# Optimization experiments

Hardware: AMD Instinct MI355X
Metric: run time of the kernel (lower is better)

The kernel has to match this reference:

```python
import jax, jax.numpy as jnp
import numpy as np

C, P, H, W, BS = 256, 2, 128, 128, 4
NH, DH = 16, 16
NPATCH = (H // P) * (W // P)   # 4096
NTOK = NPATCH + 1              # 4097 with cls token
NMASK = int((1 - 0.75) * NTOK) # 1024 kept (visible) tokens
PRED = 512
NUM_BLOCKS = 1

def _sincos_pos_embed(embed_dim, h, w):
    # faithful port of get_2d_sincos_pos_embed
    def emb1d(d, pos):
        omega = np.arange(d // 2, dtype=np.float64) / (d / 2.0)
        omega = 1.0 / 10000 ** omega
        out = np.einsum('m,d->md', pos.reshape(-1), omega)
        return np.concatenate([np.sin(out), np.cos(out)], axis=1)
    gh = np.arange(h, dtype=np.float32)
    gw = np.arange(w, dtype=np.float32)
    grid = np.stack(np.meshgrid(gw, gh), axis=0).reshape(2, 1, h, w)
    emb = np.concatenate([emb1d(embed_dim // 2, grid[0]), emb1d(embed_dim // 2, grid[1])], axis=1)
    return jnp.asarray(emb, jnp.float32)  # [h*w, embed_dim]

def _ln(x, g, b, eps=1e-5):
    mu = x.mean(-1, keepdims=True)
    var = ((x - mu) ** 2).mean(-1, keepdims=True)
    return (x - mu) * jax.lax.rsqrt(var + eps) * g + b

def _gelu(x):
    return jax.nn.gelu(x, approximate=False)  # torch nn.GELU default (erf)

def _attn(x, qkv_w, qkv_b, proj_w, proj_b, nq_g, nq_b, nk_g, nk_b):
    bs, n, c = x.shape
    qkv = x @ qkv_w + qkv_b
    q, k, v = jnp.split(qkv, 3, axis=-1)
    heads = lambda t: t.reshape(bs, n, NH, DH).transpose(0, 2, 1, 3)  # [b,h,n,d]
    q, k, v = heads(q), heads(k), heads(v)
    q = _ln(q, nq_g, nq_b)  # per-head-dim QK LayerNorm
    k = _ln(k, nk_g, nk_b)
    score = jnp.einsum('bhnd,bhmd->bhnm', q, k) / np.float32(np.sqrt(DH))
    attn = jax.nn.softmax(score, axis=-1)
    attn_map = attn.mean(axis=1)[:, 0, 1:]  # [b, n-1]
    out = jnp.einsum('bhnm,bhmd->bhnd', attn, v)
    out = out.transpose(0, 2, 1, 3).reshape(bs, n, c)
    return out @ proj_w + proj_b, attn_map

def _forward(mask_index, x, Wp, bp, cls, qkv_w, qkv_b, proj_w, proj_b, nq_g, nq_b, nk_g, nk_b,
             conv_w, conv_b, ca1_w, ca1_b, ca2_w, ca2_b, mlp1_w, mlp1_b, mlp2_w, mlp2_b,
             node_w, ln0_g, ln0_b, h1_w, h1_b, ln1_g, ln1_b, h2_w, h2_b, ln2_g, ln2_b,
             h3_w, h3_b, pr_w, pr_b):
    bs = x.shape[0]
    # PatchEmbed: conv stride=kernel=P expressed as reshape + einsum
    xp = x.reshape(bs, 3, H // P, P, W // P, P)
    tok = jnp.einsum('bchpwq,ocpq->bohw', xp, Wp) + bp[None, :, None, None]
    tok = tok.reshape(bs, C, NPATCH).transpose(0, 2, 1)  # [b, l, c]
    tok = tok + _sincos_pos_embed(C, H // P, W // P)[None]
    tok = jnp.concatenate([jnp.broadcast_to(cls, (bs, 1, C)), tok], axis=1)  # prepend cls
    # mask_img: keep NMASK tokens per the precomputed permutation prefix
    m = jnp.take_along_axis(tok, mask_index[:, :, None], axis=1)  # [b, NMASK, C]

    attn_map = None
    for blk in range(NUM_BLOCKS):
        feat = m[..., None]  # feature_list: [b, l, c, width]
        for i in range(4):
            j = blk * 4 + i
            xl = feat[..., -1]
            o1 = _gelu(xl @ conv_w[j] + conv_b[j])  # Conv1x1Act
            gate = jax.nn.sigmoid(jax.nn.relu(xl @ ca1_w[j] + ca1_b[j]) @ ca2_w[j] + ca2_b[j])
            o2 = gate * xl                           # ChannelAttention
            o4 = _gelu(xl @ mlp1_w[j] + mlp1_b[j]) @ mlp2_w[j] + mlp2_b[j]  # MLP
            cat = jnp.concatenate([feat, jnp.stack([o1, o2, xl, o4], axis=-1)], axis=-1)  # width 5+i
            wmix = jax.nn.softmax(node_w[j, :5 + i] / 0.01)
            mixed = jnp.einsum('blcn,n->blc', cat, wmix)
            a_out, attn_map = _attn(mixed, qkv_w[j], qkv_b[j], proj_w[j], proj_b[j],
                                    nq_g[j], nq_b[j], nk_g[j], nk_b[j])
            xo = a_out + mixed  # residual
            feat = jnp.concatenate([feat, xo[..., None]], axis=-1)
        m = xo
    # Predict_head (tokenwise)
    h = _ln(m, ln0_g, ln0_b)
    h = h @ h1_w + h1_b
    h = _ln(h, ln1_g, ln1_b)
    h = h @ h2_w + h2_b
    h = _ln(h, ln2_g, ln2_b)
    h = h @ h3_w + h3_b
    return h @ pr_w + pr_b  # [b, NMASK, PRED]

def setup_inputs():
    key = jax.random.key(0)
    ks = iter(jax.random.split(key, 64))
    rn = lambda shape, s=0.02: jax.random.normal(next(ks), shape, jnp.float32) * s
    noise = jax.random.normal(next(ks), (BS, NTOK))
    mask_index = jnp.argsort(noise, axis=-1)[:, :NMASK].astype(jnp.int32)
    return dict(
        x=jax.random.normal(next(ks), (BS, 3, H, W), jnp.float32),
        mask_index=mask_index,
        Wp=rn((C, 3, P, P)), bp=jnp.zeros((C,)), cls=rn((1, 1, C)),
        qkv_w=rn((4, C, 3 * C)), qkv_b=jnp.zeros((4, 3 * C)),
        proj_w=rn((4, C, C)), proj_b=jnp.zeros((4, C)),
        nq_g=jnp.ones((4, DH)), nq_b=jnp.zeros((4, DH)),
        nk_g=jnp.ones((4, DH)), nk_b=jnp.zeros((4, DH)),
        conv_w=rn((4, C, C)), conv_b=jnp.zeros((4, C)),
        ca1_w=rn((4, C, C // 16)), ca1_b=jnp.zeros((4, C // 16)),
        ca2_w=rn((4, C // 16, C)), ca2_b=jnp.zeros((4, C)),
        mlp1_w=rn((4, C, 4 * C)), mlp1_b=jnp.zeros((4, 4 * C)),
        mlp2_w=rn((4, 4 * C, C)), mlp2_b=jnp.zeros((4, C)),
        node_w=jax.random.normal(next(ks), (4, 8), jnp.float32),
        ln0_g=jnp.ones((C,)), ln0_b=jnp.zeros((C,)),
        h1_w=rn((C, 2048)), h1_b=jnp.zeros((2048,)),
        ln1_g=jnp.ones((2048,)), ln1_b=jnp.zeros((2048,)),
        h2_w=rn((2048, 256)), h2_b=jnp.zeros((256,)),
        ln2_g=jnp.ones((256,)), ln2_b=jnp.zeros((256,)),
        h3_w=rn((256, 2048)), h3_b=jnp.zeros((2048,)),
        pr_w=rn((2048, PRED)), pr_b=jnp.zeros((PRED,)),
    )

def reference(x, mask_index, Wp, bp, cls, qkv_w, qkv_b, proj_w, proj_b, nq_g, nq_b, nk_g, nk_b,
              conv_w, conv_b, ca1_w, ca1_b, ca2_w, ca2_b, mlp1_w, mlp1_b, mlp2_w, mlp2_b,
              node_w, ln0_g, ln0_b, h1_w, h1_b, ln1_g, ln1_b, h2_w, h2_b, ln2_g, ln2_b,
              h3_w, h3_b, pr_w, pr_b):
    return _forward(mask_index, x, Wp, bp, cls, qkv_w, qkv_b, proj_w, proj_b, nq_g, nq_b, nk_g, nk_b,
                    conv_w, conv_b, ca1_w, ca1_b, ca2_w, ca2_b, mlp1_w, mlp1_b, mlp2_w, mlp2_b,
                    node_w, ln0_g, ln0_b, h1_w, h1_b, ln1_g, ln1_b, h2_w, h2_b, ln2_g, ln2_b,
                    h3_w, h3_b, pr_w, pr_b)
```

## Files before the change

### kernel.cpp

```cpp
#include <hip/hip_runtime.h>
#include <math.h>
#include <cstddef>

#define RTOK 4096
#define CDIM 256
#define NHEAD 16
#define DHEAD 16
#define SEQ 1024
#define BSZ 4

#define ACT_NONE 0
#define ACT_GELU 1

typedef short short8 __attribute__((ext_vector_type(8)));
typedef float f32x4  __attribute__((ext_vector_type(4)));
typedef _Float16 half8 __attribute__((ext_vector_type(8)));
typedef _Float16 half4 __attribute__((ext_vector_type(4)));

__device__ __forceinline__ float gelu_erf(float x) {
    return 0.5f * x * (1.0f + erff(x * 0.70710678118654752f));
}
__device__ __forceinline__ unsigned short f2b(float f) {
    unsigned u = __float_as_uint(f);
    unsigned r = (u + 0x7FFFu + ((u >> 16) & 1u)) >> 16;
    return (unsigned short)r;
}
__device__ __forceinline__ float b2f(unsigned short u) {
    return __uint_as_float((unsigned)u << 16);
}
__device__ __forceinline__ void gld16(const unsigned short* g, unsigned short* l) {
    __builtin_amdgcn_global_load_lds(
        (const __attribute__((address_space(1))) unsigned int*)g,
        (__attribute__((address_space(3))) unsigned int*)l, 16, 0, 0);
}
__device__ __forceinline__ float node_wsel(const float* nwp, int cnt, int widx) {
    float ww[8];
    float mx = -1e30f;
    for (int t = 0; t < cnt; ++t) { ww[t] = nwp[t] * 100.0f; mx = fmaxf(mx, ww[t]); }
    float ssum = 0.0f;
    for (int t = 0; t < cnt; ++t) { ww[t] = expf(ww[t] - mx); ssum += ww[t]; }
    return ww[widx] / ssum;
}

struct WtSeg { const float* in; unsigned short* out; int K, N, ntx, tpz, zin, zout; };
struct WtTab { WtSeg s[9]; int cum[10]; };

__global__ __launch_bounds__(256) void wtrans_all(WtTab tab)
{
    int g = blockIdx.x;
    int si = 0;
    #pragma unroll
    for (int i = 0; i < 8; ++i) if (g >= tab.cum[i + 1]) si = i + 1;
    WtSeg sg = tab.s[si];
    int t = g - tab.cum[si];
    int z = t / sg.tpz, r = t % sg.tpz;
    int kb = (r % sg.ntx) * 32, nb = (r / sg.ntx) * 32;
    const float* in = sg.in + (size_t)z * sg.zin;
    unsigned short* out = sg.out + (size_t)z * sg.zout;

    __shared__ float tt[32][33];
    int tx = threadIdx.x & 31, ty = threadIdx.x >> 5;
    #pragma unroll
    for (int rr = 0; rr < 4; ++rr) {
        int kk = ty * 4 + rr;
        tt[kk][tx] = in[(size_t)(kb + kk) * sg.N + nb + tx];
    }
    __syncthreads();
    #pragma unroll
    for (int rr = 0; rr < 4; ++rr) {
        int nn = ty * 4 + rr;
        out[(size_t)(nb + nn) * sg.K + kb + tx] = f2b(tt[tx][nn]);
    }
}

__global__ __launch_bounds__(256) void embed_kernel(
    const float* __restrict__ x, const int* __restrict__ mask_index,
    const float* __restrict__ Wp, const float* __restrict__ bp,
    const float* __restrict__ cls,
    float* __restrict__ out, unsigned short* __restrict__ outb)
{
    int row = blockIdx.x;
    int b = row >> 10;
    int c = threadIdx.x;
    int idx = mask_index[row];
    if (idx == 0) {
        float v = cls[c];
        out[(size_t)row * 256 + c] = v;
        outb[(size_t)row * 256 + c] = f2b(v);
        return;
    }
    int p  = idx - 1;
    int ph = p >> 6, pw = p & 63;

    __shared__ float xs[12];
    if (c < 12) {
        int ch = c >> 2, r = (c >> 1) & 1, q = c & 1;
        xs[c] = x[(((size_t)b * 3 + ch) * 128 + (ph * 2 + r)) * 128 + (pw * 2 + q)];
    }
    __syncthreads();

    float acc = bp[c];
    #pragma unroll
    for (int t = 0; t < 12; ++t) acc += xs[t] * Wp[c * 12 + t];

    int part = c >> 6, cc = c & 63;
    double omega = exp((double)cc * -0.14391156831212787);
    double posv  = (part < 2) ? (double)pw : (double)ph;
    double a     = posv * omega;
    double e     = ((part & 1) == 0) ? sin(a) : cos(a);
    float v = acc + (float)e;
    out[(size_t)row * 256 + c] = v;
    outb[(size_t)row * 256 + c] = f2b(v);
}

template<int MT, int ACT, bool RES, bool FOUT, int BMODE, bool SPLIT, int NW>
__global__ __launch_bounds__(256) void gemm_mfma(
    const unsigned short* __restrict__ A, const unsigned short* __restrict__ Bt,
    const float* __restrict__ bias, const float* __restrict__ bias1,
    const float* __restrict__ Rsd,
    float* __restrict__ C, unsigned short* __restrict__ Cb,
    int M, int N, int K, int N0,
    const float* __restrict__ nwp, int ncnt, int widx)
{
    constexpr int BM = 64 * MT;
    __shared__ __align__(16) unsigned short As0[BM * 64];
    __shared__ __align__(16) unsigned short As1[BM * 64];
    __shared__ __align__(16) unsigned short Bs0[64 * 64];
    __shared__ __align__(16) unsigned short Bs1[64 * 64];
    int tid = threadIdx.x;
    int w = tid >> 6, lane = tid & 63;
    int l15 = lane & 15, q = lane >> 4;

    int gx = gridDim.x, gy = gridDim.y;
    int L = blockIdx.x + gx * blockIdx.y;
    int xcd = L & 7, j = L >> 3;
    int by = xcd * (gy >> 3) + j / gx;
    int bx = j - (j / gx) * gx;
    int row0 = by * BM, col0 = bx * 64;

    f32x4 acc[MT][4];
    #pragma unroll
    for (int mt = 0; mt < MT; ++mt)
        #pragma unroll
        for (int nt = 0; nt < 4; ++nt)
            acc[mt][nt] = (f32x4){0.f, 0.f, 0.f, 0.f};

#define G_ISSUE(AS, BS, KB)                                                   \
    do {                                                                      \
        _Pragma("unroll")                                                     \
        for (int t = 0; t < 2 * MT; ++t) {                                    \
            int slot = tid + t * 256;                                         \
            int r = slot >> 3;                                                \
            int s = (slot & 7) ^ (r & 7);                                     \
            gld16(A + (size_t)(row0 + r) * K + (KB) + s * 8, &AS[slot * 8]);  \
        }                                                                     \
        _Pragma("unroll")                                                     \
        for (int t = 0; t < 2; ++t) {                                         \
            int slot = tid + t * 256;                                         \
            int r = slot >> 3;                                                \
            int s = (slot & 7) ^ (r & 7);                                     \
            gld16(Bt + (size_t)(col0 + r) * K + (KB) + s * 8, &BS[slot * 8]); \
        }                                                                     \
    } while (0)

#define G_COMPUTE(AS, BS)                                                     \
    do {                                                                      \
        _Pragma("unroll")                                                     \
        for (int hh = 0; hh < 2; ++hh) {                                      \
            short8 af[MT];                                                    \
            _Pragma("unroll")                                                 \
            for (int mt = 0; mt < MT; ++mt) {                                 \
                int R = w * 16 * MT + mt * 16 + l15;                          \
                int c = hh * 4 + q;                                           \
                af[mt] = *(const short8*)&AS[R * 64 + ((c ^ (R & 7)) << 3)];  \
            }                                                                 \
            _Pragma("unroll")                                                 \
            for (int nt = 0; nt < 4; ++nt) {                                  \
                int R = nt * 16 + l15;                                        \
                int c = hh * 4 + q;                                           \
                short8 bf = *(const short8*)&BS[R * 64 + ((c ^ (R & 7)) << 3)];\
                _Pragma("unroll")                                             \
                for (int mt = 0; mt < MT; ++mt)                               \
                    acc[mt][nt] = __builtin_amdgcn_mfma_f32_16x16x32_bf16(    \
                        af[mt], bf, acc[mt][nt], 0, 0, 0);                    \
            }                                                                 \
        }                                                                     \
    } while (0)

    G_ISSUE(As0, Bs0, 0);
    for (int kb = 0; kb < K; kb += 128) {
        __syncthreads();
        G_ISSUE(As1, Bs1, kb + 64);
        G_COMPUTE(As0, Bs0);
        __syncthreads();
        if (kb + 128 < K) G_ISSUE(As0, Bs0, kb + 128);
        G_COMPUTE(As1, Bs1);
    }
#undef G_ISSUE
#undef G_COMPUTE

    float wsel = 0.0f;
    if (NW > 0) wsel = node_wsel(nwp, ncnt, widx);

    #pragma unroll
    for (int mt = 0; mt < MT; ++mt) {
        #pragma unroll
        for (int nt = 0; nt < 4; ++nt) {
            #pragma unroll
            for (int reg = 0; reg < 4; ++reg) {
                int row = row0 + w * 16 * MT + mt * 16 + q * 4 + reg;
                int col = col0 + nt * 16 + l15;
                if (SPLIT) {
                    float v = acc[mt][nt][reg] +
                              (col < N0 ? bias[col] : bias1[col - N0]);
                    if (ACT == ACT_GELU) v = gelu_erf(v);
                    if (col < N0) {
                        if (NW == 1) C[(size_t)row * N0 + col] += wsel * v;
                        else         C[(size_t)row * N0 + col] = v;
                    } else {
                        Cb[(size_t)row * (N - N0) + (col - N0)] = f2b(v);
                    }
                } else {
                    float v = acc[mt][nt][reg] + bias[col];
                    if (ACT == ACT_GELU) v = gelu_erf(v);
                    if (NW == 2) v = wsel * v + Rsd[(size_t)row * N + col];
                    else if (RES) v += Rsd[(size_t)row * N + col];
                    if (FOUT) C[(size_t)row * N + col] = v;
                    if (BMODE == 1) Cb[(size_t)row * N + col] = f2b(v);
                    if (BMODE == 2) {
                        _Float16 hv = (_Float16)v;
                        Cb[(size_t)row * N + col] = *(unsigned short*)&hv;
                    }
                }
            }
        }
    }
}

__global__ __launch_bounds__(256) void chanattn_kernel(
    const float* __restrict__ xl,
    const float* f0, const float* f1, const float* f2,
    const float* __restrict__ ca1w, const float* __restrict__ ca1b,
    const float* __restrict__ ca2w, const float* __restrict__ ca2b,
    const float* __restrict__ node_w, int cnt,
    float* __restrict__ MIX)
{
    __shared__ float xs[256];
    __shared__ float sm16[16];
    size_t row = blockIdx.x;
    int tid = threadIdx.x;
    xs[tid] = xl[row * 256 + tid];
    __syncthreads();

    int h = tid >> 4, part = tid & 15;
    float p = 0.f;
    #pragma unroll
    for (int i = 0; i < 16; ++i)
        p += xs[part * 16 + i] * ca1w[(part * 16 + i) * 16 + h];
    p += __shfl_down(p, 8, 16);
    p += __shfl_down(p, 4, 16);
    p += __shfl_down(p, 2, 16);
    p += __shfl_down(p, 1, 16);
    if (part == 0) sm16[h] = fmaxf(p + ca1b[h], 0.0f);
    __syncthreads();

    float g = ca2b[tid];
    #pragma unroll
    for (int hh = 0; hh < 16; ++hh) g += sm16[hh] * ca2w[hh * 256 + tid];
    g = 1.0f / (1.0f + expf(-g));
    float o2 = g * xs[tid];

    float ww[8];
    float mx = -1e30f;
    for (int t = 0; t < cnt; ++t) { ww[t] = node_w[t] * 100.0f; mx = fmaxf(mx, ww[t]); }
    float ssum = 0.0f;
    for (int t = 0; t < cnt; ++t) { ww[t] = expf(ww[t] - mx); ssum += ww[t]; }
    float inv = 1.0f / ssum;
    int j = cnt - 5;
    float acc = (ww[j] + ww[j + 3]) * inv * xs[tid] + ww[j + 2] * inv * o2;
    const float* fs[3] = {f0, f1, f2};
    for (int t = 0; t < j; ++t) acc += ww[t] * inv * fs[t][row * 256 + tid];
    MIX[row * 256 + tid] = acc;
}

__global__ __launch_bounds__(256) void ln256_kernel(
    const float* __restrict__ in, unsigned short* __restrict__ outb,
    const float* __restrict__ g, const float* __restrict__ bb)
{
    int row = blockIdx.x * 4 + (threadIdx.x >> 6);
    int lane = threadIdx.x & 63;
    f32x4 xv = *(const f32x4*)(in + (size_t)row * 256 + lane * 4);
    float s = xv[0] + xv[1] + xv[2] + xv[3];
    #pragma unroll
    for (int off = 1; off < 64; off <<= 1) s += __shfl_xor(s, off, 64);
    float mu = s * (1.0f / 256.0f);
    float d0 = xv[0]-mu, d1 = xv[1]-mu, d2 = xv[2]-mu, d3 = xv[3]-mu;
    float s2 = d0*d0 + d1*d1 + d2*d2 + d3*d3;
    #pragma unroll
    for (int off = 1; off < 64; off <<= 1) s2 += __shfl_xor(s2, off, 64);
    float rstd = rsqrtf(s2 * (1.0f / 256.0f) + 1e-5f);
    f32x4 gv = *(const f32x4*)(g + lane * 4);
    f32x4 bv = *(const f32x4*)(bb + lane * 4);
    ushort4 o;
    o.x = f2b(d0 * rstd * gv[0] + bv[0]);
    o.y = f2b(d1 * rstd * gv[1] + bv[1]);
    o.z = f2b(d2 * rstd * gv[2] + bv[2]);
    o.w = f2b(d3 * rstd * gv[3] + bv[3]);
    *(ushort4*)(outb + (size_t)row * 256 + lane * 4) = o;
}

__global__ __launch_bounds__(256) void lnwb_kernel(
    const unsigned short* __restrict__ in, unsigned short* __restrict__ outb,
    const float* __restrict__ g, const float* __restrict__ bb, int N)
{
    __shared__ float sm[4];
    size_t row = blockIdx.x;
    const unsigned short* xr = in + row * N;
    int lane = threadIdx.x & 63, wid = threadIdx.x >> 6;

    float s = 0.0f;
    for (int i = threadIdx.x; i < N; i += 256) s += b2f(xr[i]);
    #pragma unroll
    for (int off = 32; off > 0; off >>= 1) s += __shfl_down(s, off, 64);
    if (lane == 0) sm[wid] = s;
    __syncthreads();
    float mu = (sm[0] + sm[1] + sm[2] + sm[3]) / N;
    __syncthreads();

    float s2 = 0.0f;
    for (int i = threadIdx.x; i < N; i += 256) { float d = b2f(xr[i]) - mu; s2 += d * d; }
    #pragma unroll
    for (int off = 32; off > 0; off >>= 1) s2 += __shfl_down(s2, off, 64);
    if (lane == 0) sm[wid] = s2;
    __syncthreads();
    float var = (sm[0] + sm[1] + sm[2] + sm[3]) / N;
    float rstd = rsqrtf(var + 1e-5f);

    for (int i = threadIdx.x; i < N; i += 256)
        outb[row * N + i] = f2b((b2f(xr[i]) - mu) * rstd * g[i] + bb[i]);
}

__global__ __launch_bounds__(256) void attn_prep(
    const unsigned short* __restrict__ qkvh,
    const float* __restrict__ nqg, const float* __restrict__ nqb,
    const float* __restrict__ nkg, const float* __restrict__ nkb,
    unsigned short* __restrict__ Qph, unsigned short* __restrict__ Kph,
    unsigned short* __restrict__ Vph)
{
    int b = blockIdx.x >> 6;
    int tokbase = (blockIdx.x & 63) * 16;
    int tid = threadIdx.x;
    int tl = tid >> 4, h = tid & 15;
    int tok = tokbase + tl;
    const _Float16* qkv = (const _Float16*)qkvh;
    const _Float16* rowp = qkv + ((size_t)(b * 1024 + tok)) * 768;
    _Float16* Qp = (_Float16*)Qph;
    _Float16* Kp = (_Float16*)Kph;
    _Float16* Vp = (_Float16*)Vph;
    const float QSC = 0.25f * 1.44269504088896340736f;

    __shared__ _Float16 vt[16][16][17];

    {
        half8 a0 = *(const half8*)(rowp + h * 16);
        half8 a1 = *(const half8*)(rowp + h * 16 + 8);
        float v[16];
        #pragma unroll
        for (int e = 0; e < 8; ++e) { v[e] = (float)a0[e]; v[8 + e] = (float)a1[e]; }
        float mu = 0.f;
        #pragma unroll
        for (int d = 0; d < 16; ++d) mu += v[d];
        mu *= (1.0f / 16.0f);
        float var = 0.f;
        #pragma unroll
        for (int d = 0; d < 16; ++d) { float t = v[d] - mu; var += t * t; }
        var *= (1.0f / 16.0f);
        float rstd = rsqrtf(var + 1e-5f);
        half8 o0, o1;
        #pragma unroll
        for (int e = 0; e < 8; ++e) {
            o0[e] = (_Float16)(((v[e] - mu) * rstd * nqg[e] + nqb[e]) * QSC);
            o1[e] = (_Float16)(((v[8+e] - mu) * rstd * nqg[8+e] + nqb[8+e]) * QSC);
        }
        _Float16* qo = Qp + ((size_t)(b * 16 + h) * 1024 + tok) * 16;
        *(half8*)qo = o0;
        *(half8*)(qo + 8) = o1;
    }
    {
        half8 a0 = *(const half8*)(rowp + 256 + h * 16);
        half8 a1 = *(const half8*)(rowp + 256 + h * 16 + 8);
        float v[16];
        #pragma unroll
        for (int e = 0; e < 8; ++e) { v[e] = (float)a0[e]; v[8 + e] = (float)a1[e]; }
        float mu = 0.f;
        #pragma unroll
        for (int d = 0; d < 16; ++d) mu += v[d];
        mu *= (1.0f / 16.0f);
        float var = 0.f;
        #pragma unroll
        for (int d = 0; d < 16; ++d) { float t = v[d] - mu; var += t * t; }
        var *= (1.0f / 16.0f);
        float rstd = rsqrtf(var + 1e-5f);
        half8 o0, o1;
        #pragma unroll
        for (int e = 0; e < 8; ++e) {
            o0[e] = (_Float16)((v[e] - mu) * rstd * nkg[e] + nkb[e]);
            o1[e] = (_Float16)((v[8+e] - mu) * rstd * nkg[8+e] + nkb[8+e]);
        }
        _Float16* ko = Kp + ((size_t)(b * 16 + h) * 1024 + tok) * 16;
        *(half8*)ko = o0;
        *(half8*)(ko + 8) = o1;
    }
    {
        half8 a0 = *(const half8*)(rowp + 512 + h * 16);
        half8 a1 = *(const half8*)(rowp + 512 + h * 16 + 8);
        #pragma unroll
        for (int e = 0; e < 8; ++e) { vt[tl][h][e] = a0[e]; vt[tl][h][8 + e] = a1[e]; }
    }
    __syncthreads();
    {
        int h2 = tid >> 4, d = tid & 15;
        half8 o0, o1;
        #pragma unroll
        for (int t = 0; t < 8; ++t) { o0[t] = vt[t][h2][d]; o1[t] = vt[8 + t][h2][d]; }
        _Float16* vo = Vp + ((size_t)(b * 16 + h2) * 16 + d) * 1024 + tokbase;
        *(half8*)vo = o0;
        *(half8*)(vo + 8) = o1;
    }
}

__global__ __launch_bounds__(256) void attn_kernel(
    const unsigned short* __restrict__ Qph, const unsigned short* __restrict__ Kph,
    const unsigned short* __restrict__ Vph,
    unsigned short* __restrict__ outb)
{
    int qt = blockIdx.x, h = blockIdx.y, b = blockIdx.z;
    int bh = b * 16 + h;
    int tid = threadIdx.x;
    int w = tid >> 6, lane = tid & 63;
    int l15 = lane & 15, quad = lane >> 4;
    const _Float16* Qp = (const _Float16*)Qph + (size_t)bh * 1024 * 16;
    const _Float16* Kp = (const _Float16*)Kph + (size_t)bh * 1024 * 16;
    const _Float16* Vp = (const _Float16*)Vph + (size_t)bh * 16 * 1024;

    __shared__ __align__(16) _Float16 Qs[64 * 40];
    __shared__ __align__(16) _Float16 Kb[128 * 40];
    __shared__ __align__(16) _Float16 Vt[16 * 136];
    __shared__ __align__(16) _Float16 Ps[4][16 * 136];

    uint4 z4 = {0, 0, 0, 0};
    if (tid < 64) {
        *(uint4*)&Qs[tid * 40 + 16] = z4;
        *(uint4*)&Qs[tid * 40 + 24] = z4;
    } else if (tid < 192) {
        int r = tid - 64;
        *(uint4*)&Kb[r * 40 + 16] = z4;
        *(uint4*)&Kb[r * 40 + 24] = z4;
    }
    if (tid < 128) {
        int r = tid >> 1, part = tid & 1;
        *(uint4*)&Qs[r * 40 + part * 8] =
            *(const uint4*)(Qp + (size_t)(qt * 64 + r) * 16 + part * 8);
    }
    __syncthreads();

    half8 bq = *(const half8*)&Qs[(w * 16 + l15) * 40 + quad * 8];
    float mst = -1e30f, lst = 0.f;
    f32x4 acco = (f32x4){0.f, 0.f, 0.f, 0.f};

    for (int kt = 0; kt < 8; ++kt) {
        __syncthreads();
        {
            int r = tid >> 1, part = tid & 1;
            *(uint4*)&Kb[r * 40 + part * 8] =
                *(const uint4*)(Kp + (size_t)(kt * 128 + r) * 16 + part * 8);
        }
        {
            int d = tid >> 4, kk8 = tid & 15;
            *(uint4*)&Vt[d * 136 + kk8 * 8] =
                *(const uint4*)(Vp + (size_t)d * 1024 + kt * 128 + kk8 * 8);
        }
        __syncthreads();

        f32x4 sacc[8];
        #pragma unroll
        for (int ni = 0; ni < 8; ++ni) {
            half8 ak = *(const half8*)&Kb[(ni * 16 + l15) * 40 + quad * 8];
            sacc[ni] = __builtin_amdgcn_mfma_f32_16x16x32_f16(
                ak, bq, (f32x4){0.f, 0.f, 0.f, 0.f}, 0, 0, 0);
        }
        half8 bv[4];
        #pragma unroll
        for (int c = 0; c < 4; ++c)
            bv[c] = *(const half8*)&Vt[l15 * 136 + c * 32 + quad * 8];

        float rm = sacc[0][0];
        #pragma unroll
        for (int ni = 0; ni < 8; ++ni)
            #pragma unroll
            for (int reg = 0; reg < 4; ++reg)
                rm = fmaxf(rm, sacc[ni][reg]);
        rm = fmaxf(rm, __shfl_xor(rm, 16, 64));
        rm = fmaxf(rm, __shfl_xor(rm, 32, 64));
        float mn  = fmaxf(mst, rm);
        float cor = exp2f(mst - mn);
        mst = mn;
        lst *= cor;
        #pragma unroll
        for (int reg = 0; reg < 4; ++reg) {
            float cR = __shfl(cor, (lane & 48) + quad * 4 + reg, 64);
            acco[reg] *= cR;
        }
        float lsum = 0.f;
        #pragma unroll
        for (int ni = 0; ni < 8; ++ni) {
            half4 ph;
            #pragma unroll
            for (int reg = 0; reg < 4; ++reg) {
                float p = exp2f(sacc[ni][reg] - mn);
                lsum += p;
                ph[reg] = (_Float16)p;
            }
            *(half4*)&Ps[w][l15 * 136 + ni * 16 + quad * 4] = ph;
        }
        lsum += __shfl_xor(lsum, 16, 64);
        lsum += __shfl_xor(lsum, 32, 64);
        lst += lsum;

        #pragma unroll
        for (int c = 0; c < 4; ++c) {
            half8 p0 = *(const half8*)&Ps[w][l15 * 136 + c * 32 + quad * 8];
            acco = __builtin_amdgcn_mfma_f32_16x16x32_f16(p0, bv[c], acco, 0, 0, 0);
        }
    }

    #pragma unroll
    for (int reg = 0; reg < 4; ++reg) {
        float lR = __shfl(lst, (lane & 48) + quad * 4 + reg, 64);
        float o = acco[reg] / lR;
        int row = b * 1024 + qt * 64 + w * 16 + quad * 4 + reg;
        outb[(size_t)row * 256 + h * 16 + l15] = f2b(o);
    }
}

extern "C" void kernel_launch(void* const* d_in, const int* in_sizes, int n_in,
                              void* d_out, int out_size, void* d_ws, size_t ws_size,
                              hipStream_t stream)
{
    const float* x          = (const float*)d_in[0];
    const int*   mask_index = (const int*)  d_in[1];
    const float* Wp         = (const float*)d_in[2];
    const float* bp         = (const float*)d_in[3];
    const float* cls        = (const float*)d_in[4];
    const float* qkv_w      = (const float*)d_in[5];
    const float* qkv_b      = (const float*)d_in[6];
    const float* proj_w     = (const float*)d_in[7];
    const float* proj_b     = (const float*)d_in[8];
    const float* nq_g       = (const float*)d_in[9];
    const float* nq_b       = (const float*)d_in[10];
    const float* nk_g       = (const float*)d_in[11];
    const float* nk_b       = (const float*)d_in[12];
    const float* conv_w     = (const float*)d_in[13];
    const float* conv_b     = (const float*)d_in[14];
    const float* ca1_w      = (const float*)d_in[15];
    const float* ca1_b      = (const float*)d_in[16];
    const float* ca2_w      = (const float*)d_in[17];
    const float* ca2_b      = (const float*)d_in[18];
    const float* mlp1_w     = (const float*)d_in[19];
    const float* mlp1_b     = (const float*)d_in[20];
    const float* mlp2_w     = (const float*)d_in[21];
    const float* mlp2_b     = (const float*)d_in[22];
    const float* node_w     = (const float*)d_in[23];
    const float* ln0_g      = (const float*)d_in[24];
    const float* ln0_b      = (const float*)d_in[25];
    const float* h1_w       = (const float*)d_in[26];
    const float* h1_b       = (const float*)d_in[27];
    const float* ln1_g      = (const float*)d_in[28];
    const float* ln1_b      = (const float*)d_in[29];
    const float* h2_w       = (const float*)d_in[30];
    const float* h2_b       = (const float*)d_in[31];
    const float* ln2_g      = (const float*)d_in[32];
    const float* ln2_b      = (const float*)d_in[33];
    const float* h3_w       = (const float*)d_in[34];
    const float* h3_b       = (const float*)d_in[35];
    const float* pr_w       = (const float*)d_in[36];
    const float* pr_b       = (const float*)d_in[37];
    float* out = (float*)d_out;

    char* base = (char*)d_ws;
    size_t off = 0;
    auto alloc = [&](size_t bytes) -> char* {
        char* p = base + off;
        off += (bytes + 255) & ~(size_t)255;
        return p;
    };
    const size_t RC = (size_t)RTOK * CDIM;
    float* F[5];
    unsigned short* Fb[5];
    for (int i = 0; i < 5; ++i) F[i] = (float*)alloc(RC * 4);
    for (int i = 0; i < 5; ++i) Fb[i] = (unsigned short*)alloc(RC * 2);
    float* MIX = (float*)alloc(RC * 4);
    unsigned short* MIXb = (unsigned short*)alloc(RC * 2);
    unsigned short* AOb  = (unsigned short*)alloc(RC * 2);
    unsigned short* BIGH = (unsigned short*)alloc((size_t)RTOK * 768 * 2);
    unsigned short* Qp   = (unsigned short*)alloc(RC * 2);
    unsigned short* Kp   = (unsigned short*)alloc(RC * 2);
    unsigned short* Vp   = (unsigned short*)alloc(RC * 2);
    unsigned short* H1b  = (unsigned short*)alloc((size_t)RTOK * 2048 * 2);
    unsigned short* MIDU = (unsigned short*)alloc((size_t)RTOK * 2048 * 2);
    unsigned short* L0b  = (unsigned short*)alloc(RC * 2);
    unsigned short* L2b  = (unsigned short*)alloc(RC * 2);
    unsigned short* H3b  = (unsigned short*)alloc((size_t)RTOK * 2048 * 2);
    unsigned short* cm1b  = (unsigned short*)alloc((size_t)4 * 1280 * 256 * 2);
    unsigned short* qkvb  = (unsigned short*)alloc((size_t)4 * 768 * 256 * 2);
    unsigned short* projb = (unsigned short*)alloc((size_t)4 * 256 * 256 * 2);
    unsigned short* mlp2b = (unsigned short*)alloc((size_t)4 * 256 * 1024 * 2);
    unsigned short* h1b   = (unsigned short*)alloc((size_t)2048 * 256 * 2);
    unsigned short* h2b   = (unsigned short*)alloc((size_t)256 * 2048 * 2);
    unsigned short* h3b   = (unsigned short*)alloc((size_t)2048 * 256 * 2);
    unsigned short* prb   = (unsigned short*)alloc((size_t)512 * 2048 * 2);

    {
        WtTab tab;
        int c = 0, idx = 0;
        auto seg = [&](const float* in, unsigned short* outp, int K, int N,
                       int z, int zin, int zout) {
            WtSeg s; s.in = in; s.out = outp; s.K = K; s.N = N;
            s.ntx = K / 32; s.tpz = (K / 32) * (N / 32);
            s.zin = zin; s.zout = zout;
            tab.s[idx] = s; tab.cum[idx] = c;
            c += s.tpz * z; ++idx;
        };
        seg(conv_w, cm1b,         256, 256,  4, 256 * 256,  1280 * 256);
        seg(mlp1_w, cm1b + 65536, 256, 1024, 4, 256 * 1024, 1280 * 256);
        seg(qkv_w,  qkvb,  256, 768,  4, 256 * 768,  768 * 256);
        seg(proj_w, projb, 256, 256,  4, 256 * 256,  256 * 256);
        seg(mlp2_w, mlp2b, 1024, 256, 4, 1024 * 256, 256 * 1024);
        seg(h1_w, h1b, 256, 2048, 1, 0, 0);
        seg(h2_w, h2b, 2048, 256, 1, 0, 0);
        seg(h3_w, h3b, 256, 2048, 1, 0, 0);
        seg(pr_w, prb, 2048, 512, 1, 0, 0);
        tab.cum[9] = c;
        wtrans_all<<<c, 256, 0, stream>>>(tab);
    }

    embed_kernel<<<RTOK, 256, 0, stream>>>(x, mask_index, Wp, bp, cls, F[0], Fb[0]);

    for (int j = 0; j < 4; ++j) {
        const float* xl = F[j];
        const unsigned short* xlb = Fb[j];
        chanattn_kernel<<<RTOK, 256, 0, stream>>>(
            xl, F[0], F[1], F[2],
            ca1_w + (size_t)j * 256 * 16, ca1_b + j * 16,
            ca2_w + (size_t)j * 16 * 256, ca2_b + j * 256,
            node_w + j * 8, 5 + j, MIX);
        gemm_mfma<2, ACT_GELU, false, false, 0, true, 1><<<dim3(20, 32), 256, 0, stream>>>(
            xlb, cm1b + (size_t)j * 1280 * 256, conv_b + j * 256, mlp1_b + j * 1024,
            nullptr, MIX, MIDU, RTOK, 1280, 256, 256, node_w + j * 8, 5 + j, j + 1);
        gemm_mfma<1, ACT_NONE, false, true, 1, false, 2><<<dim3(4, 64), 256, 0, stream>>>(
            MIDU, mlp2b + (size_t)j * 256 * 1024, mlp2_b + j * 256, nullptr, MIX,
            MIX, MIXb, RTOK, 256, 1024, 0, node_w + j * 8, 5 + j, j + 4);
        gemm_mfma<2, ACT_NONE, false, false, 2, false, 0><<<dim3(12, 32), 256, 0, stream>>>(
            MIXb, qkvb + (size_t)j * 768 * 256, qkv_b + j * 768, nullptr, nullptr,
            nullptr, BIGH, RTOK, 768, 256, 0, nullptr, 0, 0);
        attn_prep<<<256, 256, 0, stream>>>(
            BIGH, nq_g + j * 16, nq_b + j * 16, nk_g + j * 16, nk_b + j * 16,
            Qp, Kp, Vp);
        attn_kernel<<<dim3(16, NHEAD, BSZ), 256, 0, stream>>>(Qp, Kp, Vp, AOb);
        gemm_mfma<1, ACT_NONE, true, true, 1, false, 0><<<dim3(4, 64), 256, 0, stream>>>(
            AOb, projb + (size_t)j * 256 * 256, proj_b + j * 256, nullptr, MIX,
            F[j + 1], Fb[j + 1], RTOK, 256, 256, 0, nullptr, 0, 0);
    }

    ln256_kernel<<<1024, 256, 0, stream>>>(F[4], L0b, ln0_g, ln0_b);
    gemm_mfma<2, ACT_NONE, false, false, 1, false, 0><<<dim3(32, 32), 256, 0, stream>>>(
        L0b, h1b, h1_b, nullptr, nullptr, nullptr, H1b, RTOK, 2048, 256, 0,
        nullptr, 0, 0);
    lnwb_kernel<<<RTOK, 256, 0, stream>>>(H1b, MIDU, ln1_g, ln1_b, 2048);
    gemm_mfma<1, ACT_NONE, false, true, 0, false, 0><<<dim3(4, 64), 256, 0, stream>>>(
        MIDU, h2b, h2_b, nullptr, nullptr, MIX, nullptr, RTOK, 256, 2048, 0,
        nullptr, 0, 0);
    ln256_kernel<<<1024, 256, 0, stream>>>(MIX, L2b, ln2_g, ln2_b);
    gemm_mfma<2, ACT_NONE, false, false, 1, false, 0><<<dim3(32, 32), 256, 0, stream>>>(
        L2b, h3b, h3_b, nullptr, nullptr, nullptr, H3b, RTOK, 2048, 256, 0,
        nullptr, 0, 0);
    gemm_mfma<1, ACT_NONE, false, true, 0, false, 0><<<dim3(8, 64), 256, 0, stream>>>(
        H3b, prb, pr_b, nullptr, nullptr, out, nullptr, RTOK, 512, 2048, 0,
        nullptr, 0, 0);
}
```

Measured before the change: 671.6 us.

## Merge setup kernels, fuse conv/mlp1 GEMM with channel attention, pipeline attention loads

Merges the weight-transpose and embedding kernels into one launch. It also runs the conv+mlp1 GEMM and the channel-attention kernel as two block ranges of a single launch, writing the conv branch to a separate O1 buffer that the mlp2 GEMM epilogue folds into MIX. The LayerNorm over 2048 columns now uses one wavefront per row with vector loads and shuffle reductions. The attention kernel double-buffers K/V tiles in registers and LDS and switches QK to the 16x16x16 f16 MFMA with compact layouts. These changes aim to cut launch count, serial dependencies and LDS sync stalls, at the cost of an extra fp32 buffer and more epilogue reads.

```diff
diff --git a/kernel.cpp b/kernel.cpp
--- a/kernel.cpp
+++ b/kernel.cpp
@@ -45,72 +45,68 @@
 struct WtSeg { const float* in; unsigned short* out; int K, N, ntx, tpz, zin, zout; };
 struct WtTab { WtSeg s[9]; int cum[10]; };
 
-__global__ __launch_bounds__(256) void wtrans_all(WtTab tab)
-{
-    int g = blockIdx.x;
-    int si = 0;
-    #pragma unroll
-    for (int i = 0; i < 8; ++i) if (g >= tab.cum[i + 1]) si = i + 1;
-    WtSeg sg = tab.s[si];
-    int t = g - tab.cum[si];
-    int z = t / sg.tpz, r = t % sg.tpz;
-    int kb = (r % sg.ntx) * 32, nb = (r / sg.ntx) * 32;
-    const float* in = sg.in + (size_t)z * sg.zin;
-    unsigned short* out = sg.out + (size_t)z * sg.zout;
-
-    __shared__ float tt[32][33];
-    int tx = threadIdx.x & 31, ty = threadIdx.x >> 5;
-    #pragma unroll
-    for (int rr = 0; rr < 4; ++rr) {
-        int kk = ty * 4 + rr;
-        tt[kk][tx] = in[(size_t)(kb + kk) * sg.N + nb + tx];
-    }
-    __syncthreads();
-    #pragma unroll
-    for (int rr = 0; rr < 4; ++rr) {
-        int nn = ty * 4 + rr;
-        out[(size_t)(nb + nn) * sg.K + kb + tx] = f2b(tt[tx][nn]);
-    }
-}
-
-__global__ __launch_bounds__(256) void embed_kernel(
+__global__ __launch_bounds__(256) void setup_kernel(
+    WtTab tab,
     const float* __restrict__ x, const int* __restrict__ mask_index,
     const float* __restrict__ Wp, const float* __restrict__ bp,
     const float* __restrict__ cls,
-    float* __restrict__ out, unsigned short* __restrict__ outb)
+    float* __restrict__ Fout, unsigned short* __restrict__ Fbout)
 {
-    int row = blockIdx.x;
-    int b = row >> 10;
-    int c = threadIdx.x;
-    int idx = mask_index[row];
-    if (idx == 0) {
-        float v = cls[c];
-        out[(size_t)row * 256 + c] = v;
-        outb[(size_t)row * 256 + c] = f2b(v);
-        return;
-    }
-    int p  = idx - 1;
-    int ph = p >> 6, pw = p & 63;
-
+    __shared__ float tt[32][33];
     __shared__ float xs[12];
-    if (c < 12) {
-        int ch = c >> 2, r = (c >> 1) & 1, q = c & 1;
-        xs[c] = x[(((size_t)b * 3 + ch) * 128 + (ph * 2 + r)) * 128 + (pw * 2 + q)];
-    }
-    __syncthreads();
-
-    float acc = bp[c];
-    #pragma unroll
-    for (int t = 0; t < 12; ++t) acc += xs[t] * Wp[c * 12 + t];
-
-    int part = c >> 6, cc = c & 63;
-    double omega = exp((double)cc * -0.14391156831212787);
-    double posv  = (part < 2) ? (double)pw : (double)ph;
-    double a     = posv * omega;
-    double e     = ((part & 1) == 0) ? sin(a) : cos(a);
-    float v = acc + (float)e;
-    out[(size_t)row * 256 + c] = v;
-    outb[(size_t)row * 256 + c] = f2b(v);
+    if ((int)blockIdx.x < tab.cum[9]) {
+        int g = blockIdx.x;
+        int si = 0;
+        #pragma unroll
+        for (int i = 0; i < 8; ++i) if (g >= tab.cum[i + 1]) si = i + 1;
+        WtSeg sg = tab.s[si];
+        int t = g - tab.cum[si];
+        int z = t / sg.tpz, r = t % sg.tpz;
+        int kb = (r % sg.ntx) * 32, nb = (r / sg.ntx) * 32;
+        const float* in = sg.in + (size_t)z * sg.zin;
+        unsigned short* out = sg.out + (size_t)z * sg.zout;
+        int tx = threadIdx.x & 31, ty = threadIdx.x >> 5;
+        #pragma unroll
+        for (int rr = 0; rr < 4; ++rr) {
+            int kk = ty * 4 + rr;
+            tt[kk][tx] = in[(size_t)(kb + kk) * sg.N + nb + tx];
+        }
+        __syncthreads();
+        #pragma unroll
+        for (int rr = 0; rr < 4; ++rr) {
+            int nn = ty * 4 + rr;
+            out[(size_t)(nb + nn) * sg.K + kb + tx] = f2b(tt[tx][nn]);
+        }
+    } else {
+        int row = blockIdx.x - tab.cum[9];
+        int b = row >> 10;
+        int c = threadIdx.x;
+        int idx = mask_index[row];
+        if (idx == 0) {
+            float v = cls[c];
+            Fout[(size_t)row * 256 + c] = v;
+            Fbout[(size_t)row * 256 + c] = f2b(v);
+            return;
+        }
+        int p  = idx - 1;
+        int ph = p >> 6, pw = p & 63;
+        if (c < 12) {
+            int ch = c >> 2, r = (c >> 1) & 1, q = c & 1;
+            xs[c] = x[(((size_t)b * 3 + ch) * 128 + (ph * 2 + r)) * 128 + (pw * 2 + q)];
+        }
+        __syncthreads();
+        float acc = bp[c];
+        #pragma unroll
+        for (int t = 0; t < 12; ++t) acc += xs[t] * Wp[c * 12 + t];
+        int part = c >> 6, cc = c & 63;
+        double omega = exp((double)cc * -0.14391156831212787);
+        double posv  = (part < 2) ? (double)pw : (double)ph;
+        double a     = posv * omega;
+        double e     = ((part & 1) == 0) ? sin(a) : cos(a);
+        float v = acc + (float)e;
+        Fout[(size_t)row * 256 + c] = v;
+        Fbout[(size_t)row * 256 + c] = f2b(v);
+    }
 }
 
 template<int MT, int ACT, bool RES, bool FOUT, int BMODE, bool SPLIT, int NW>
@@ -120,7 +116,8 @@
     const float* __restrict__ Rsd,
     float* __restrict__ C, unsigned short* __restrict__ Cb,
     int M, int N, int K, int N0,
-    const float* __restrict__ nwp, int ncnt, int widx)
+    const float* __restrict__ nwp, int ncnt, int widx,
+    const float* __restrict__ O1p, int widxB)
 {
     constexpr int BM = 64 * MT;
     __shared__ __align__(16) unsigned short As0[BM * 64];
@@ -199,8 +196,9 @@
 #undef G_ISSUE
 #undef G_COMPUTE
 
-    float wsel = 0.0f;
+    float wsel = 0.0f, wselB = 0.0f;
     if (NW > 0) wsel = node_wsel(nwp, ncnt, widx);
+    if (NW == 4) wselB = node_wsel(nwp, ncnt, widxB);
 
     #pragma unroll
     for (int mt = 0; mt < MT; ++mt) {
@@ -214,16 +212,14 @@
                     float v = acc[mt][nt][reg] +
                               (col < N0 ? bias[col] : bias1[col - N0]);
                     if (ACT == ACT_GELU) v = gelu_erf(v);
-                    if (col < N0) {
-                        if (NW == 1) C[(size_t)row * N0 + col] += wsel * v;
-                        else         C[(size_t)row * N0 + col] = v;
-                    } else {
-                        Cb[(size_t)row * (N - N0) + (col - N0)] = f2b(v);
-                    }
+                    if (col < N0) C[(size_t)row * N0 + col] = v;
+                    else Cb[(size_t)row * (N - N0) + (col - N0)] = f2b(v);
                 } else {
                     float v = acc[mt][nt][reg] + bias[col];
                     if (ACT == ACT_GELU) v = gelu_erf(v);
                     if (NW == 2) v = wsel * v + Rsd[(size_t)row * N + col];
+                    else if (NW == 4) v = wsel * v + Rsd[(size_t)row * N + col]
+                                        + wselB * O1p[(size_t)row * N + col];
                     else if (RES) v += Rsd[(size_t)row * N + col];
                     if (FOUT) C[(size_t)row * N + col] = v;
                     if (BMODE == 1) Cb[(size_t)row * N + col] = f2b(v);
@@ -237,7 +233,10 @@
     }
 }
 
-__global__ __launch_bounds__(256) void chanattn_kernel(
+__global__ __launch_bounds__(256) void cm1chan_kernel(
+    const unsigned short* __restrict__ A, const unsigned short* __restrict__ Bt,
+    const float* __restrict__ biasC, const float* __restrict__ biasM,
+    float* __restrict__ O1, unsigned short* __restrict__ MIDU,
     const float* __restrict__ xl,
     const float* f0, const float* f1, const float* f2,
     const float* __restrict__ ca1w, const float* __restrict__ ca1b,
@@ -245,42 +244,138 @@
     const float* __restrict__ node_w, int cnt,
     float* __restrict__ MIX)
 {
+    __shared__ __align__(16) unsigned short As0[128 * 64];
+    __shared__ __align__(16) unsigned short As1[128 * 64];
+    __shared__ __align__(16) unsigned short Bs0[64 * 64];
+    __shared__ __align__(16) unsigned short Bs1[64 * 64];
     __shared__ float xs[256];
     __shared__ float sm16[16];
-    size_t row = blockIdx.x;
     int tid = threadIdx.x;
-    xs[tid] = xl[row * 256 + tid];
-    __syncthreads();
-
-    int h = tid >> 4, part = tid & 15;
-    float p = 0.f;
-    #pragma unroll
-    for (int i = 0; i < 16; ++i)
-        p += xs[part * 16 + i] * ca1w[(part * 16 + i) * 16 + h];
-    p += __shfl_down(p, 8, 16);
-    p += __shfl_down(p, 4, 16);
-    p += __shfl_down(p, 2, 16);
-    p += __shfl_down(p, 1, 16);
-    if (part == 0) sm16[h] = fmaxf(p + ca1b[h], 0.0f);
-    __syncthreads();
-
-    float g = ca2b[tid];
-    #pragma unroll
-    for (int hh = 0; hh < 16; ++hh) g += sm16[hh] * ca2w[hh * 256 + tid];
-    g = 1.0f / (1.0f + expf(-g));
-    float o2 = g * xs[tid];
-
-    float ww[8];
-    float mx = -1e30f;
-    for (int t = 0; t < cnt; ++t) { ww[t] = node_w[t] * 100.0f; mx = fmaxf(mx, ww[t]); }
-    float ssum = 0.0f;
-    for (int t = 0; t < cnt; ++t) { ww[t] = expf(ww[t] - mx); ssum += ww[t]; }
-    float inv = 1.0f / ssum;
-    int j = cnt - 5;
-    float acc = (ww[j] + ww[j + 3]) * inv * xs[tid] + ww[j + 2] * inv * o2;
-    const float* fs[3] = {f0, f1, f2};
-    for (int t = 0; t < j; ++t) acc += ww[t] * inv * fs[t][row * 256 + tid];
-    MIX[row * 256 + tid] = acc;
+
+    if ((int)blockIdx.x < 640) {
+        const int K = 256, N0 = 256;
+        int w = tid >> 6, lane = tid & 63;
+        int l15 = lane & 15, q = lane >> 4;
+        int L = blockIdx.x;
+        int xcd = L & 7, j = L >> 3;
+        int by = xcd * 4 + j / 20;
+        int bx = j - (j / 20) * 20;
+        int row0 = by * 128, col0 = bx * 64;
+
+        f32x4 acc[2][4];
+        #pragma unroll
+        for (int mt = 0; mt < 2; ++mt)
+            #pragma unroll
+            for (int nt = 0; nt < 4; ++nt)
+                acc[mt][nt] = (f32x4){0.f, 0.f, 0.f, 0.f};
+
+#define C_ISSUE(AS, BS, KB)                                                   \
+    do {                                                                      \
+        _Pragma("unroll")                                                     \
+        for (int t = 0; t < 4; ++t) {                                         \
+            int slot = tid + t * 256;                                         \
+            int r = slot >> 3;                                                \
+            int s = (slot & 7) ^ (r & 7);                                     \
+            gld16(A + (size_t)(row0 + r) * K + (KB) + s * 8, &AS[slot * 8]);  \
+        }                                                                     \
+        _Pragma("unroll")                                                     \
+        for (int t = 0; t < 2; ++t) {                                         \
+            int slot = tid + t * 256;                                         \
+            int r = slot >> 3;                                                \
+            int s = (slot & 7) ^ (r & 7);                                     \
+            gld16(Bt + (size_t)(col0 + r) * K + (KB) + s * 8, &BS[slot * 8]); \
+        }                                                                     \
+    } while (0)
+
+#define C_COMPUTE(AS, BS)                                                     \
+    do {                                                                      \
+        _Pragma("unroll")                                                     \
+        for (int hh = 0; hh < 2; ++hh) {                                      \
+            short8 af[2];                                                     \
+            _Pragma("unroll")                                                 \
+            for (int mt = 0; mt < 2; ++mt) {                                  \
+                int R = w * 32 + mt * 16 + l15;                               \
+                int c = hh * 4 + q;                                           \
+                af[mt] = *(const short8*)&AS[R * 64 + ((c ^ (R & 7)) << 3)];  \
+            }                                                                 \
+            _Pragma("unroll")                                                 \
+            for (int nt = 0; nt < 4; ++nt) {                                  \
+                int R = nt * 16 + l15;                                        \
+                int c = hh * 4 + q;                                           \
+                short8 bf = *(const short8*)&BS[R * 64 + ((c ^ (R & 7)) << 3)];\
+                _Pragma("unroll")                                             \
+                for (int mt = 0; mt < 2; ++mt)                                \
+                    acc[mt][nt] = __builtin_amdgcn_mfma_f32_16x16x32_bf16(    \
+                        af[mt], bf, acc[mt][nt], 0, 0, 0);                    \
+            }                                                                 \
+        }                                                                     \
+    } while (0)
+
+        C_ISSUE(As0, Bs0, 0);
+        for (int kb = 0; kb < K; kb += 128) {
+            __syncthreads();
+            C_ISSUE(As1, Bs1, kb + 64);
+            C_COMPUTE(As0, Bs0);
+            __syncthreads();
+            if (kb + 128 < K) C_ISSUE(As0, Bs0, kb + 128);
+            C_COMPUTE(As1, Bs1);
+        }
+#undef C_ISSUE
+#undef C_COMPUTE
+
+        #pragma unroll
+        for (int mt = 0; mt < 2; ++mt) {
+            #pragma unroll
+            for (int nt = 0; nt < 4; ++nt) {
+                #pragma unroll
+                for (int reg = 0; reg < 4; ++reg) {
+                    int row = row0 + w * 32 + mt * 16 + q * 4 + reg;
+                    int col = col0 + nt * 16 + l15;
+                    if (col < N0) {
+                        float v = gelu_erf(acc[mt][nt][reg] + biasC[col]);
+                        O1[(size_t)row * 256 + col] = v;
+                    } else {
+                        float v = gelu_erf(acc[mt][nt][reg] + biasM[col - 256]);
+                        MIDU[(size_t)row * 1024 + (col - 256)] = f2b(v);
+                    }
+                }
+            }
+        }
+    } else {
+        size_t row = blockIdx.x - 640;
+        xs[tid] = xl[row * 256 + tid];
+        __syncthreads();
+
+        int h = tid >> 4, part = tid & 15;
+        float p = 0.f;
+        #pragma unroll
+        for (int i = 0; i < 16; ++i)
+            p += xs[part * 16 + i] * ca1w[(part * 16 + i) * 16 + h];
+        p += __shfl_down(p, 8, 16);
+        p += __shfl_down(p, 4, 16);
+        p += __shfl_down(p, 2, 16);
+        p += __shfl_down(p, 1, 16);
+        if (part == 0) sm16[h] = fmaxf(p + ca1b[h], 0.0f);
+        __syncthreads();
+
+        float g = ca2b[tid];
+        #pragma unroll
+        for (int hh = 0; hh < 16; ++hh) g += sm16[hh] * ca2w[hh * 256 + tid];
+        g = 1.0f / (1.0f + expf(-g));
+        float o2 = g * xs[tid];
+
+        float ww[8];
+        float mx = -1e30f;
+        for (int t = 0; t < cnt; ++t) { ww[t] = node_w[t] * 100.0f; mx = fmaxf(mx, ww[t]); }
+        float ssum = 0.0f;
+        for (int t = 0; t < cnt; ++t) { ww[t] = expf(ww[t] - mx); ssum += ww[t]; }
+        float inv = 1.0f / ssum;
+        int jj = cnt - 5;
+        float acc2 = (ww[jj] + ww[jj + 3]) * inv * xs[tid] + ww[jj + 2] * inv * o2;
+        const float* fs[3] = {f0, f1, f2};
+        for (int t = 0; t < jj; ++t) acc2 += ww[t] * inv * fs[t][row * 256 + tid];
+        MIX[row * 256 + tid] = acc2;
+    }
 }
 
 __global__ __launch_bounds__(256) void ln256_kernel(
@@ -309,35 +404,39 @@
     *(ushort4*)(outb + (size_t)row * 256 + lane * 4) = o;
 }
 
-__global__ __launch_bounds__(256) void lnwb_kernel(
+__global__ __launch_bounds__(256) void ln2048w_kernel(
     const unsigned short* __restrict__ in, unsigned short* __restrict__ outb,
-    const float* __restrict__ g, const float* __restrict__ bb, int N)
+    const float* __restrict__ g, const float* __restrict__ bb)
 {
-    __shared__ float sm[4];
-    size_t row = blockIdx.x;
-    const unsigned short* xr = in + row * N;
-    int lane = threadIdx.x & 63, wid = threadIdx.x >> 6;
-
-    float s = 0.0f;
-    for (int i = threadIdx.x; i < N; i += 256) s += b2f(xr[i]);
-    #pragma unroll
-    for (int off = 32; off > 0; off >>= 1) s += __shfl_down(s, off, 64);
-    if (lane == 0) sm[wid] = s;
-    __syncthreads();
-    float mu = (sm[0] + sm[1] + sm[2] + sm[3]) / N;
-    __syncthreads();
-
-    float s2 = 0.0f;
-    for (int i = threadIdx.x; i < N; i += 256) { float d = b2f(xr[i]) - mu; s2 += d * d; }
-    #pragma unroll
-    for (int off = 32; off > 0; off >>= 1) s2 += __shfl_down(s2, off, 64);
-    if (lane == 0) sm[wid] = s2;
-    __syncthreads();
-    float var = (sm[0] + sm[1] + sm[2] + sm[3]) / N;
-    float rstd = rsqrtf(var + 1e-5f);
-
-    for (int i = threadIdx.x; i < N; i += 256)
-        outb[row * N + i] = f2b((b2f(xr[i]) - mu) * rstd * g[i] + bb[i]);
+    int row = blockIdx.x * 4 + (threadIdx.x >> 6);
+    int lane = threadIdx.x & 63;
+    const unsigned short* xr = in + (size_t)row * 2048 + lane * 32;
+    unsigned short v[32];
+    *(uint4*)&v[0]  = *(const uint4*)&xr[0];
+    *(uint4*)&v[8]  = *(const uint4*)&xr[8];
+    *(uint4*)&v[16] = *(const uint4*)&xr[16];
+    *(uint4*)&v[24] = *(const uint4*)&xr[24];
+    float s = 0.f;
+    #pragma unroll
+    for (int i = 0; i < 32; ++i) s += b2f(v[i]);
+    #pragma unroll
+    for (int off = 1; off < 64; off <<= 1) s += __shfl_xor(s, off, 64);
+    float mu = s * (1.0f / 2048.0f);
+    float s2 = 0.f;
+    #pragma unroll
+    for (int i = 0; i < 32; ++i) { float d = b2f(v[i]) - mu; s2 += d * d; }
+    #pragma unroll
+    for (int off = 1; off < 64; off <<= 1) s2 += __shfl_xor(s2, off, 64);
+    float rstd = rsqrtf(s2 * (1.0f / 2048.0f) + 1e-5f);
+    unsigned short o[32];
+    #pragma unroll
+    for (int i = 0; i < 32; ++i)
+        o[i] = f2b((b2f(v[i]) - mu) * rstd * g[lane * 32 + i] + bb[lane * 32 + i]);
+    unsigned short* op = outb + (size_t)row * 2048 + lane * 32;
+    *(uint4*)&op[0]  = *(const uint4*)&o[0];
+    *(uint4*)&op[8]  = *(const uint4*)&o[8];
+    *(uint4*)&op[16] = *(const uint4*)&o[16];
+    *(uint4*)&op[24] = *(const uint4*)&o[24];
 }
 
 __global__ __launch_bounds__(256) void attn_prep(
@@ -443,56 +542,65 @@
     const _Float16* Kp = (const _Float16*)Kph + (size_t)bh * 1024 * 16;
     const _Float16* Vp = (const _Float16*)Vph + (size_t)bh * 16 * 1024;
 
-    __shared__ __align__(16) _Float16 Qs[64 * 40];
-    __shared__ __align__(16) _Float16 Kb[128 * 40];
-    __shared__ __align__(16) _Float16 Vt[16 * 136];
+    __shared__ __align__(16) _Float16 Qs[64 * 16];
+    __shared__ __align__(16) _Float16 Kb[2][128 * 16];
+    __shared__ __align__(16) _Float16 Vt[2][16 * 136];
     __shared__ __align__(16) _Float16 Ps[4][16 * 136];
 
-    uint4 z4 = {0, 0, 0, 0};
-    if (tid < 64) {
-        *(uint4*)&Qs[tid * 40 + 16] = z4;
-        *(uint4*)&Qs[tid * 40 + 24] = z4;
-    } else if (tid < 192) {
-        int r = tid - 64;
-        *(uint4*)&Kb[r * 40 + 16] = z4;
-        *(uint4*)&Kb[r * 40 + 24] = z4;
-    }
     if (tid < 128) {
         int r = tid >> 1, part = tid & 1;
-        *(uint4*)&Qs[r * 40 + part * 8] =
+        *(uint4*)&Qs[r * 16 + part * 8] =
             *(const uint4*)(Qp + (size_t)(qt * 64 + r) * 16 + part * 8);
     }
+
+    uint4 r0, r1;
+#define A_LOAD(KT)                                                            \
+    do {                                                                      \
+        if (tid < 128) {                                                      \
+            const uint4* src = (const uint4*)(Kp + (size_t)((KT) * 128 + tid) * 16); \
+            r0 = src[0]; r1 = src[1];                                         \
+        } else {                                                              \
+            int t = tid - 128, d = t >> 3, k8 = t & 7;                        \
+            const uint4* src = (const uint4*)(Vp + (size_t)d * 1024 + (KT) * 128 + k8 * 16); \
+            r0 = src[0]; r1 = src[1];                                         \
+        }                                                                     \
+    } while (0)
+#define A_WRITE(BUF)                                                          \
+    do {                                                                      \
+        if (tid < 128) {                                                      \
+            *(uint4*)&Kb[BUF][tid * 16 + 0] = r0;                             \
+            *(uint4*)&Kb[BUF][tid * 16 + 8] = r1;                             \
+        } else {                                                              \
+            int t = tid - 128, d = t >> 3, k8 = t & 7;                        \
+            *(uint4*)&Vt[BUF][d * 136 + k8 * 16 + 0] = r0;                    \
+            *(uint4*)&Vt[BUF][d * 136 + k8 * 16 + 8] = r1;                    \
+        }                                                                     \
+    } while (0)
+
+    A_LOAD(0);
+    A_WRITE(0);
     __syncthreads();
 
-    half8 bq = *(const half8*)&Qs[(w * 16 + l15) * 40 + quad * 8];
+    half4 bq = *(const half4*)&Qs[(w * 16 + l15) * 16 + quad * 4];
     float mst = -1e30f, lst = 0.f;
     f32x4 acco = (f32x4){0.f, 0.f, 0.f, 0.f};
 
+    int p = 0;
     for (int kt = 0; kt < 8; ++kt) {
-        __syncthreads();
-        {
-            int r = tid >> 1, part = tid & 1;
-            *(uint4*)&Kb[r * 40 + part * 8] =
-                *(const uint4*)(Kp + (size_t)(kt * 128 + r) * 16 + part * 8);
-        }
-        {
-            int d = tid >> 4, kk8 = tid & 15;
-            *(uint4*)&Vt[d * 136 + kk8 * 8] =
-                *(const uint4*)(Vp + (size_t)d * 1024 + kt * 128 + kk8 * 8);
-        }
-        __syncthreads();
+        if (kt < 7) A_LOAD(kt + 1);
+        if (kt > 0) __syncthreads();
 
         f32x4 sacc[8];
         #pragma unroll
         for (int ni = 0; ni < 8; ++ni) {
-            half8 ak = *(const half8*)&Kb[(ni * 16 + l15) * 40 + quad * 8];
-            sacc[ni] = __builtin_amdgcn_mfma_f32_16x16x32_f16(
+            half4 ak = *(const half4*)&Kb[p][(ni * 16 + l15) * 16 + quad * 4];
+            sacc[ni] = __builtin_amdgcn_mfma_f32_16x16x16f16(
                 ak, bq, (f32x4){0.f, 0.f, 0.f, 0.f}, 0, 0, 0);
         }
         half8 bv[4];
         #pragma unroll
         for (int c = 0; c < 4; ++c)
-            bv[c] = *(const half8*)&Vt[l15 * 136 + c * 32 + quad * 8];
+            bv[c] = *(const half8*)&Vt[p][l15 * 136 + c * 32 + quad * 8];
 
         float rm = sacc[0][0];
         #pragma unroll
@@ -517,9 +625,9 @@
             half4 ph;
             #pragma unroll
             for (int reg = 0; reg < 4; ++reg) {
-                float p = exp2f(sacc[ni][reg] - mn);
-                lsum += p;
-                ph[reg] = (_Float16)p;
+                float pp = exp2f(sacc[ni][reg] - mn);
+                lsum += pp;
+                ph[reg] = (_Float16)pp;
             }
             *(half4*)&Ps[w][l15 * 136 + ni * 16 + quad * 4] = ph;
         }
@@ -532,7 +640,12 @@
             half8 p0 = *(const half8*)&Ps[w][l15 * 136 + c * 32 + quad * 8];
             acco = __builtin_amdgcn_mfma_f32_16x16x32_f16(p0, bv[c], acco, 0, 0, 0);
         }
-    }
+
+        if (kt < 7) A_WRITE(1 - p);
+        p ^= 1;
+    }
+#undef A_LOAD
+#undef A_WRITE
 
     #pragma unroll
     for (int reg = 0; reg < 4; ++reg) {
@@ -600,6 +713,7 @@
     for (int i = 0; i < 5; ++i) F[i] = (float*)alloc(RC * 4);
     for (int i = 0; i < 5; ++i) Fb[i] = (unsigned short*)alloc(RC * 2);
     float* MIX = (float*)alloc(RC * 4);
+    float* O1  = (float*)alloc(RC * 4);
     unsigned short* MIXb = (unsigned short*)alloc(RC * 2);
     unsigned short* AOb  = (unsigned short*)alloc(RC * 2);
     unsigned short* BIGH = (unsigned short*)alloc((size_t)RTOK * 768 * 2);
@@ -641,50 +755,48 @@
         seg(h3_w, h3b, 256, 2048, 1, 0, 0);
         seg(pr_w, prb, 2048, 512, 1, 0, 0);
         tab.cum[9] = c;
-        wtrans_all<<<c, 256, 0, stream>>>(tab);
-    }
-
-    embed_kernel<<<RTOK, 256, 0, stream>>>(x, mask_index, Wp, bp, cls, F[0], Fb[0]);
+        setup_kernel<<<c + RTOK, 256, 0, stream>>>(
+            tab, x, mask_index, Wp, bp, cls, F[0], Fb[0]);
+    }
 
     for (int j = 0; j < 4; ++j) {
         const float* xl = F[j];
         const unsigned short* xlb = Fb[j];
-        chanattn_kernel<<<RTOK, 256, 0, stream>>>(
+        cm1chan_kernel<<<640 + RTOK, 256, 0, stream>>>(
+            xlb, cm1b + (size_t)j * 1280 * 256, conv_b + j * 256, mlp1_b + j * 1024,
+            O1, MIDU,
             xl, F[0], F[1], F[2],
             ca1_w + (size_t)j * 256 * 16, ca1_b + j * 16,
             ca2_w + (size_t)j * 16 * 256, ca2_b + j * 256,
             node_w + j * 8, 5 + j, MIX);
-        gemm_mfma<2, ACT_GELU, false, false, 0, true, 1><<<dim3(20, 32), 256, 0, stream>>>(
-            xlb, cm1b + (size_t)j * 1280 * 256, conv_b + j * 256, mlp1_b + j * 1024,
-            nullptr, MIX, MIDU, RTOK, 1280, 256, 256, node_w + j * 8, 5 + j, j + 1);
-        gemm_mfma<1, ACT_NONE, false, true, 1, false, 2><<<dim3(4, 64), 256, 0, stream>>>(
+        gemm_mfma<1, ACT_NONE, false, true, 1, false, 4><<<dim3(4, 64), 256, 0, stream>>>(
             MIDU, mlp2b + (size_t)j * 256 * 1024, mlp2_b + j * 256, nullptr, MIX,
-            MIX, MIXb, RTOK, 256, 1024, 0, node_w + j * 8, 5 + j, j + 4);
+            MIX, MIXb, RTOK, 256, 1024, 0, node_w + j * 8, 5 + j, j + 4, O1, j + 1);
         gemm_mfma<2, ACT_NONE, false, false, 2, false, 0><<<dim3(12, 32), 256, 0, stream>>>(
             MIXb, qkvb + (size_t)j * 768 * 256, qkv_b + j * 768, nullptr, nullptr,
-            nullptr, BIGH, RTOK, 768, 256, 0, nullptr, 0, 0);
+            nullptr, BIGH, RTOK, 768, 256, 0, nullptr, 0, 0, nullptr, 0);
         attn_prep<<<256, 256, 0, stream>>>(
             BIGH, nq_g + j * 16, nq_b + j * 16, nk_g + j * 16, nk_b + j * 16,
             Qp, Kp, Vp);
         attn_kernel<<<dim3(16, NHEAD, BSZ), 256, 0, stream>>>(Qp, Kp, Vp, AOb);
         gemm_mfma<1, ACT_NONE, true, true, 1, false, 0><<<dim3(4, 64), 256, 0, stream>>>(
             AOb, projb + (size_t)j * 256 * 256, proj_b + j * 256, nullptr, MIX,
-            F[j + 1], Fb[j + 1], RTOK, 256, 256, 0, nullptr, 0, 0);
+            F[j + 1], Fb[j + 1], RTOK, 256, 256, 0, nullptr, 0, 0, nullptr, 0);
     }
 
     ln256_kernel<<<1024, 256, 0, stream>>>(F[4], L0b, ln0_g, ln0_b);
     gemm_mfma<2, ACT_NONE, false, false, 1, false, 0><<<dim3(32, 32), 256, 0, stream>>>(
         L0b, h1b, h1_b, nullptr, nullptr, nullptr, H1b, RTOK, 2048, 256, 0,
-        nullptr, 0, 0);
-    lnwb_kernel<<<RTOK, 256, 0, stream>>>(H1b, MIDU, ln1_g, ln1_b, 2048);
+        nullptr, 0, 0, nullptr, 0);
+    ln2048w_kernel<<<1024, 256, 0, stream>>>(H1b, MIDU, ln1_g, ln1_b);
     gemm_mfma<1, ACT_NONE, false, true, 0, false, 0><<<dim3(4, 64), 256, 0, stream>>>(
         MIDU, h2b, h2_b, nullptr, nullptr, MIX, nullptr, RTOK, 256, 2048, 0,
-        nullptr, 0, 0);
+        nullptr, 0, 0, nullptr, 0);
     ln256_kernel<<<1024, 256, 0, stream>>>(MIX, L2b, ln2_g, ln2_b);
     gemm_mfma<2, ACT_NONE, false, false, 1, false, 0><<<dim3(32, 32), 256, 0, stream>>>(
         L2b, h3b, h3_b, nullptr, nullptr, nullptr, H3b, RTOK, 2048, 256, 0,
-        nullptr, 0, 0);
+        nullptr, 0, 0, nullptr, 0);
     gemm_mfma<1, ACT_NONE, false, true, 0, false, 0><<<dim3(8, 64), 256, 0, stream>>>(
         H3b, prb, pr_b, nullptr, nullptr, out, nullptr, RTOK, 512, 2048, 0,
-        nullptr, 0, 0);
-}
+        nullptr, 0, 0, nullptr, 0);
+}
```

New measurement: 681.4 us. No clear change (+1.5%).
